# Performance work log

Hardware: AMD Instinct MI355X
Metric: run time of the kernel (lower is better)

## Reference

```python
import jax, jax.numpy as jnp
import numpy as np

EMBEDDING_DIM = 256
NUM_EMBEDDINGS = 8192
COMMITMENT_COST = 0.25
DECAY = 0.99
EPSILON = 1e-5


def setup_inputs() -> dict:
    key = jax.random.key(0)
    k1, k2 = jax.random.split(key)
    inputs = jax.random.normal(k1, (16, 32, 32, EMBEDDING_DIM), dtype=jnp.float32)
    # VarianceScaling(distribution='uniform'), fan_in scaling over [D, K]
    limit = float(np.sqrt(3.0 / EMBEDDING_DIM))
    embeddings = jax.random.uniform(k2, (EMBEDDING_DIM, NUM_EMBEDDINGS),
                                    minval=-limit, maxval=limit, dtype=jnp.float32)
    return {
        'inputs': inputs,
        'embeddings': embeddings,
        'ema_cs_hidden': jnp.zeros((NUM_EMBEDDINGS,), jnp.float32),
        'ema_dw_hidden': embeddings,  # hk initializes ema_dw to the embeddings
        'counter': 0,
        'is_training': 1,
    }


def reference(inputs, embeddings, ema_cs_hidden, ema_dw_hidden, counter, is_training):
    flat = inputs.reshape(-1, EMBEDDING_DIM)                        # [N, D]
    distances = (jnp.sum(flat ** 2, axis=1, keepdims=True)
                 - 2.0 * (flat @ embeddings)
                 + jnp.sum(embeddings ** 2, axis=0, keepdims=True))  # [N, K]
    encoding_indices = jnp.argmax(-distances, axis=1)                # [N]
    encodings = jax.nn.one_hot(encoding_indices, NUM_EMBEDDINGS,
                               dtype=distances.dtype)                # [N, K]
    idx = encoding_indices.reshape(inputs.shape[:-1])
    quantized = embeddings.T[idx]                                    # gather codebook
    e_latent_loss = jnp.mean((jax.lax.stop_gradient(quantized) - inputs) ** 2)
    loss = COMMITMENT_COST * e_latent_loss

    if is_training:
        # haiku ExponentialMovingAverage with zero-debias
        new_counter = counter + 1
        debias = 1.0 - DECAY ** new_counter
        cs_hidden = ema_cs_hidden * DECAY + jnp.sum(encodings, axis=0) * (1.0 - DECAY)
        cs_avg = cs_hidden / debias                                  # [K]
        dw = flat.T @ encodings                                      # [D, K] scatter-add as GEMM
        dw_hidden = ema_dw_hidden * DECAY + dw * (1.0 - DECAY)
        dw_avg = dw_hidden / debias
        n = jnp.sum(cs_avg)
        cs_norm = (cs_avg + EPSILON) / (n + NUM_EMBEDDINGS * EPSILON) * n
        new_embeddings = dw_avg / cs_norm[None, :]                   # [D, K]
    else:
        new_embeddings = embeddings

    # straight-through estimator
    quantized_st = inputs + jax.lax.stop_gradient(quantized - inputs)
    avg_probs = jnp.mean(encodings, axis=0)
    perplexity = jnp.exp(-jnp.sum(avg_probs * jnp.log(avg_probs + 1e-10)))
    return (quantized_st, loss, perplexity, idx, new_embeddings)
```

## Files before the change

kernel.cpp:

```cpp
#include <hip/hip_runtime.h>
#include <math.h>

#define DD 256
#define KK 8192
#define NN 16384
#define DECAYF 0.99f
#define EPSF 1e-5f
#define TAU 4e-3f

#define O_Q    0
#define O_LOSS 4194304
#define O_PERP 4194305
#define O_IDX  4194306
#define O_EMB  4210690

typedef float f32x4 __attribute__((ext_vector_type(4)));
typedef _Float16 f16x8 __attribute__((ext_vector_type(8)));

__device__ __forceinline__ unsigned short f2h(float f) {
  union { _Float16 h; unsigned short u; } c;
  c.h = (_Float16)f;
  return c.u;
}

__device__ __forceinline__ void gll16(const void* g, void* l) {
  __builtin_amdgcn_global_load_lds((const __attribute__((address_space(1))) void*)g,
                                   (__attribute__((address_space(3))) void*)l, 16, 0, 0);
}

__global__ void k_convert_x(const float* __restrict__ x, unsigned short* __restrict__ Ah,
                            float* __restrict__ esq) {
  int i = blockIdx.x * 256 + threadIdx.x;
  if (blockIdx.x < 32) esq[blockIdx.x * 256 + threadIdx.x] = 0.f;
  float4 v = ((const float4*)x)[i];
  ushort4 h;
  h.x = f2h(v.x); h.y = f2h(v.y); h.z = f2h(v.z); h.w = f2h(v.w);
  ((ushort4*)Ah)[i] = h;
}

__global__ void k_convert_e(const float* __restrict__ emb, unsigned short* __restrict__ Eh,
                            float* __restrict__ embT, float* __restrict__ esq) {
  __shared__ float ld[32 * 33];
  int t = threadIdx.x;
  int k0 = blockIdx.x * 32, d0 = blockIdx.y * 32;
  {
    int din = t >> 3, kq = (t & 7) * 4;
    float4 v = *(const float4*)(emb + (size_t)(d0 + din) * KK + k0 + kq);
    ld[din * 33 + kq + 0] = v.x; ld[din * 33 + kq + 1] = v.y;
    ld[din * 33 + kq + 2] = v.z; ld[din * 33 + kq + 3] = v.w;
  }
  __syncthreads();
  int kout = t >> 3, dq = (t & 7) * 4;
  float f0 = ld[(dq + 0) * 33 + kout], f1 = ld[(dq + 1) * 33 + kout];
  float f2 = ld[(dq + 2) * 33 + kout], f3 = ld[(dq + 3) * 33 + kout];
  size_t o = (size_t)(k0 + kout) * DD + d0 + dq;
  float4 fv; fv.x = f0; fv.y = f1; fv.z = f2; fv.w = f3;
  *(float4*)(embT + o) = fv;
  ushort4 hv;
  hv.x = f2h(f0); hv.y = f2h(f1); hv.z = f2h(f2); hv.w = f2h(f3);
  *(ushort4*)(Eh + o) = hv;
  float p = (f0 * f0 + f1 * f1) + (f2 * f2 + f3 * f3);
  p += __shfl_xor(p, 1, 64);
  p += __shfl_xor(p, 2, 64);
  p += __shfl_xor(p, 4, 64);
  if ((t & 7) == 0) atomicAdd(esq + k0 + kout, p);
}

__global__ void k_zero(float4* __restrict__ p) {
  p[(size_t)blockIdx.x * 256 + threadIdx.x] = make_float4(0.f, 0.f, 0.f, 0.f);
}

__launch_bounds__(256, 2)
__global__ void k_dist_mfma(const unsigned short* __restrict__ Ah, const unsigned short* __restrict__ Bh,
                            const float* __restrict__ esq,
                            float* __restrict__ part1, float* __restrict__ part2,
                            int* __restrict__ partidx) {
  __shared__ __align__(16) unsigned short sA[8192];
  __shared__ __align__(16) unsigned short sB[8192];

  const int tid = threadIdx.x;
  const int w = tid >> 6, lane = tid & 63;
  const int kb = blockIdx.x, nb = blockIdx.y;
  const int row0 = nb * 128, col0 = kb * 128;

  size_t gA[4], gB[4];
  int lbase[4];
  #pragma unroll
  for (int s = 0; s < 4; ++s) {
    int r = (w * 4 + s) * 8 + (lane >> 3);
    int c = (lane & 7) ^ (r & 7);
    gA[s] = (size_t)(row0 + r) * DD + c * 8;
    gB[s] = (size_t)(col0 + r) * DD + c * 8;
    lbase[s] = (w * 4 + s) * 512;
  }
  const int m = lane & 15, q = lane >> 4;

  f32x4 acc[2][8];
  #pragma unroll
  for (int i = 0; i < 2; ++i)
    #pragma unroll
    for (int j = 0; j < 8; ++j) acc[i][j] = (f32x4)0.f;

  for (int it = 0; it < 4; ++it) {
    const int d0 = it * 64;
    __syncthreads();
    #pragma unroll
    for (int s = 0; s < 4; ++s) {
      gll16(Ah + gA[s] + d0, sA + lbase[s]);
      gll16(Bh + gB[s] + d0, sB + lbase[s]);
    }
    __syncthreads();
    #pragma unroll
    for (int kk = 0; kk < 2; ++kk) {
      f16x8 a[2];
      #pragma unroll
      for (int i = 0; i < 2; ++i) {
        int wr = w * 32 + i * 16 + m;
        int slot = (kk * 4 + q) ^ (wr & 7);
        a[i] = *(const f16x8*)(sA + wr * 64 + slot * 8);
      }
      #pragma unroll
      for (int j = 0; j < 8; ++j) {
        int cn = j * 16 + m;
        int slot = (kk * 4 + q) ^ (cn & 7);
        f16x8 b = *(const f16x8*)(sB + cn * 64 + slot * 8);
        acc[0][j] = __builtin_amdgcn_mfma_f32_16x16x32_f16(a[0], b, acc[0][j], 0, 0, 0);
        acc[1][j] = __builtin_amdgcn_mfma_f32_16x16x32_f16(a[1], b, acc[1][j], 0, 0, 0);
      }
    }
  }

  float eq[8];
  #pragma unroll
  for (int j = 0; j < 8; ++j) eq[j] = esq[col0 + j * 16 + m];

  #pragma unroll
  for (int i = 0; i < 2; ++i) {
    #pragma unroll
    for (int reg = 0; reg < 4; ++reg) {
      float m1 = 3.402823466e+38f, m2 = 3.402823466e+38f;
      int bi = 0;
      #pragma unroll
      for (int j = 0; j < 8; ++j) {
        float dd = fmaf(-2.0f, acc[i][j][reg], eq[j]);
        if (dd < m1) { m2 = m1; m1 = dd; bi = col0 + j * 16 + m; }
        else if (dd < m2) m2 = dd;
      }
      #pragma unroll
      for (int st = 1; st < 16; st <<= 1) {
        float ov = __shfl_xor(m1, st, 64);
        int   oi = __shfl_xor(bi, st, 64);
        float o2 = __shfl_xor(m2, st, 64);
        float big = fmaxf(m1, ov);
        m2 = fminf(fminf(m2, o2), big);
        if (ov < m1 || (ov == m1 && oi < bi)) { m1 = ov; bi = oi; }
      }
      if (m == 0) {
        int prow = row0 + w * 32 + i * 16 + q * 4 + reg;
        int pidx = prow * 64 + kb;
        part1[pidx] = m1; part2[pidx] = m2; partidx[pidx] = bi;
      }
    }
  }
}

__global__ void k_argmin2(const float* __restrict__ part1, const float* __restrict__ part2,
                          const int* __restrict__ partidx, int* __restrict__ idxw,
                          int* __restrict__ listc, int* __restrict__ list) {
  int w = threadIdx.x >> 6, l = threadIdx.x & 63;
  int row = blockIdx.x * 4 + w;
  int base = row * 64 + l;
  float m1 = part1[base], m2 = part2[base];
  int bi = partidx[base];
  #pragma unroll
  for (int st = 1; st < 64; st <<= 1) {
    float ov = __shfl_xor(m1, st, 64);
    int   oi = __shfl_xor(bi, st, 64);
    float o2 = __shfl_xor(m2, st, 64);
    float big = fmaxf(m1, ov);
    m2 = fminf(fminf(m2, o2), big);
    if (ov < m1 || (ov == m1 && oi < bi)) { m1 = ov; bi = oi; }
  }
  if (l == 0) {
    idxw[row] = bi;
    if (m2 - m1 < TAU) { int pos = atomicAdd(listc, 1); list[pos] = row; }
  }
}

__global__ void k_rescore(const float* __restrict__ x, const float* __restrict__ emb,
                          const int* __restrict__ listc, const int* __restrict__ list,
                          unsigned long long* __restrict__ keys) {
  __shared__ float se[8192];
  __shared__ double red[256];
  const int t = threadIdx.x;
  const int k0 = blockIdx.x * 32;
  #pragma unroll
  for (int i = 0; i < 32; ++i) {
    int elem = i * 256 + t;
    int d = elem >> 5, c = elem & 31;
    se[d * 32 + c] = emb[(size_t)d * KK + k0 + c];
  }
  __syncthreads();
  const int c = t & 31, p = t >> 5;
  int cnt = *listc;
  for (int li = blockIdx.y; li < cnt; li += gridDim.y) {
    int row = list[li];
    const float* xr = x + (size_t)row * DD;
    double acc = 0.0;
    #pragma unroll
    for (int j = 0; j < 32; ++j) {
      int d = p * 32 + j;
      double df = (double)xr[d] - (double)se[d * 32 + c];
      acc = fma(df, df, acc);
    }
    red[c * 8 + p] = acc;
    __syncthreads();
    if (t < 64) {
      unsigned long long key = ~0ull;
      if (t < 32) {
        double dist = 0.0;
        #pragma unroll
        for (int qq = 0; qq < 8; ++qq) dist += red[t * 8 + qq];
        key = ((unsigned long long)__double_as_longlong(dist) & ~0x1FFFull)
              | (unsigned long long)(k0 + t);
      }
      #pragma unroll
      for (int s = 1; s < 64; s <<= 1) {
        unsigned long long o = __shfl_xor(key, s, 64);
        if (o < key) key = o;
      }
      if (t == 0) atomicMin(&keys[row], key);
    }
    __syncthreads();
  }
}

__global__ void k_gather(const float* __restrict__ x, const float* __restrict__ embT,
                         const int* __restrict__ idxw, const unsigned long long* __restrict__ keys,
                         const int* __restrict__ train,
                         float* __restrict__ outq, float* __restrict__ outidx,
                         float* __restrict__ dwT, float* __restrict__ counts,
                         float* __restrict__ loss_part) {
  int w = threadIdx.x >> 6, l = threadIdx.x & 63;
  int n = blockIdx.x * 4 + w;
  unsigned long long kv = keys[n];
  int k = (kv != ~0ull) ? (int)(kv & 0x1FFFull) : idxw[n];
  float4 xv = ((const float4*)(x + (size_t)n * DD))[l];
  float4 qv = ((const float4*)(embT + (size_t)k * DD))[l];
  int d = l * 4;

  ((float4*)(outq + (size_t)n * DD))[l] = qv;

  float e0 = qv.x - xv.x, e1 = qv.y - xv.y, e2 = qv.z - xv.z, e3 = qv.w - xv.w;
  float ls = (e0 * e0 + e1 * e1) + (e2 * e2 + e3 * e3);

  if (*train) {
    const float wdw = 1.0f - DECAYF;
    float* base = dwT + (size_t)k * DD + d;
    atomicAdd(base + 0, xv.x * wdw);
    atomicAdd(base + 1, xv.y * wdw);
    atomicAdd(base + 2, xv.z * wdw);
    atomicAdd(base + 3, xv.w * wdw);
  }

  #pragma unroll
  for (int s = 1; s < 64; s <<= 1) ls += __shfl_xor(ls, s, 64);
  if (l == 0) {
    atomicAdd(&loss_part[blockIdx.x & 255], ls);
    atomicAdd(&counts[k], 1.0f);
    outidx[n] = (float)k;
  }
}

__global__ void k_stats(const float* __restrict__ counts, const float* __restrict__ ema_cs,
                        const int* __restrict__ counter, const int* __restrict__ train,
                        const float* __restrict__ loss_part, float* __restrict__ csn,
                        float* __restrict__ outloss, float* __restrict__ outperp) {
  __shared__ float s_n[4], s_e[4], s_l[4], s_tot[1];
  int tid = threadIdx.x;
  float debias = 1.0f - powf(DECAYF, (float)(*counter + 1));
  float nloc = 0.f, eloc = 0.f;
  float lloc = loss_part[tid];
  float avg[32];
  for (int i = 0; i < 32; ++i) {
    int k = tid + i * 256;
    float c = counts[k];
    float h = ema_cs[k] * DECAYF + c * (1.0f - DECAYF);
    float a = h / debias;
    avg[i] = a;
    nloc += a;
    float p = c * (1.0f / 16384.0f);
    eloc += p * logf(p + 1e-10f);
  }
  #pragma unroll
  for (int s = 1; s < 64; s <<= 1) {
    nloc += __shfl_xor(nloc, s, 64);
    eloc += __shfl_xor(eloc, s, 64);
    lloc += __shfl_xor(lloc, s, 64);
  }
  int w = tid >> 6, lane = tid & 63;
  if (lane == 0) { s_n[w] = nloc; s_e[w] = eloc; s_l[w] = lloc; }
  __syncthreads();
  if (tid == 0) {
    float nt = (s_n[0] + s_n[1]) + (s_n[2] + s_n[3]);
    float et = (s_e[0] + s_e[1]) + (s_e[2] + s_e[3]);
    float lt = (s_l[0] + s_l[1]) + (s_l[2] + s_l[3]);
    s_tot[0] = nt;
    outperp[0] = expf(-et);
    outloss[0] = 0.25f * (lt / 4194304.0f);
  }
  __syncthreads();
  float nsum = s_tot[0];
  float denom = nsum + 8192.0f * EPSF;
  for (int i = 0; i < 32; ++i) {
    int k = tid + i * 256;
    csn[k] = (avg[i] + EPSF) / denom * nsum;
  }
}

__global__ void k_final(const float* __restrict__ dwT, const float* __restrict__ ema_dw,
                        const float* __restrict__ emb, const float* __restrict__ csn,
                        const int* __restrict__ counter, const int* __restrict__ train,
                        float* __restrict__ out4) {
  __shared__ float ld[32 * 33];
  int t = threadIdx.x;
  int k0 = blockIdx.x * 32, d0 = blockIdx.y * 32;
  if (*train) {
    {
      int ki = t >> 3, dq = (t & 7) * 4;
      float4 v = *(const float4*)(dwT + (size_t)(k0 + ki) * DD + d0 + dq);
      ld[ki * 33 + dq + 0] = v.x; ld[ki * 33 + dq + 1] = v.y;
      ld[ki * 33 + dq + 2] = v.z; ld[ki * 33 + dq + 3] = v.w;
    }
    __syncthreads();
    int dout = t >> 3, kq = (t & 7) * 4;
    size_t o = (size_t)(d0 + dout) * KK + k0 + kq;
    float4 e = *(const float4*)(ema_dw + o);
    float4 c = *(const float4*)(csn + k0 + kq);
    float inv = 1.0f / (1.0f - powf(DECAYF, (float)(*counter + 1)));
    float4 r;
    r.x = fmaf(e.x, DECAYF, ld[(kq + 0) * 33 + dout]) * inv / c.x;
    r.y = fmaf(e.y, DECAYF, ld[(kq + 1) * 33 + dout]) * inv / c.y;
    r.z = fmaf(e.z, DECAYF, ld[(kq + 2) * 33 + dout]) * inv / c.z;
    r.w = fmaf(e.w, DECAYF, ld[(kq + 3) * 33 + dout]) * inv / c.w;
    *(float4*)(out4 + o) = r;
  } else {
    int dout = t >> 3, kq = (t & 7) * 4;
    size_t o = (size_t)(d0 + dout) * KK + k0 + kq;
    *(float4*)(out4 + o) = *(const float4*)(emb + o);
  }
}

extern "C" void kernel_launch(void* const* d_in, const int* in_sizes, int n_in,
                              void* d_out, int out_size, void* d_ws, size_t ws_size,
                              hipStream_t stream) {
  (void)in_sizes; (void)n_in; (void)out_size; (void)ws_size;
  const float* x      = (const float*)d_in[0];
  const float* emb    = (const float*)d_in[1];
  const float* ema_cs = (const float*)d_in[2];
  const float* ema_dw = (const float*)d_in[3];
  const int*   counter = (const int*)d_in[4];
  const int*   train   = (const int*)d_in[5];

  float* out = (float*)d_out;
  float* outq    = out + O_Q;
  float* outloss = out + O_LOSS;
  float* outperp = out + O_PERP;
  float* outidx  = out + O_IDX;
  float* out4    = out + O_EMB;

  char* W = (char*)d_ws;
  unsigned short* Ah   = (unsigned short*)(W);
  unsigned short* Eh   = (unsigned short*)(W + 8388608);
  float* embT          = (float*)(W + 12582912);
  float* part1         = (float*)(W + 20971520);
  float* part2         = (float*)(W + 25165824);
  int*   partidx       = (int*)(W + 29360128);
  float* dwT           = part1;
  unsigned long long* keys = (unsigned long long*)(W + 33554432);
  float* esq           = (float*)(W + 33685504);
  float* csn           = (float*)(W + 33718272);
  float* counts        = (float*)(W + 33751040);
  float* loss_part     = (float*)(W + 33783808);
  int*   listc         = (int*)(W + 33784832);
  int*   list          = (int*)(W + 33784836);
  int*   idxw          = (int*)(W + 33850372);

  hipMemsetAsync(counts, 0, 32768 + 1024 + 4, stream);
  hipMemsetAsync(keys, 0xFF, NN * sizeof(unsigned long long), stream);

  k_convert_x<<<4096, 256, 0, stream>>>(x, Ah, esq);
  k_convert_e<<<dim3(256, 8), 256, 0, stream>>>(emb, Eh, embT, esq);
  k_dist_mfma<<<dim3(64, 128), 256, 0, stream>>>(Ah, Eh, esq, part1, part2, partidx);
  k_argmin2<<<4096, 256, 0, stream>>>(part1, part2, partidx, idxw, listc, list);
  k_zero<<<2048, 256, 0, stream>>>((float4*)dwT);
  k_rescore<<<dim3(256, 8), 256, 0, stream>>>(x, emb, listc, list, keys);
  k_gather<<<4096, 256, 0, stream>>>(x, embT, idxw, keys, train, outq, outidx, dwT, counts, loss_part);
  k_stats<<<1, 256, 0, stream>>>(counts, ema_cs, counter, train, loss_part, csn, outloss, outperp);
  k_final<<<dim3(256, 8), 256, 0, stream>>>(dwT, ema_dw, emb, csn, counter, train, out4);
}
```

Before: 400.7 us.

## Fuse conversion kernels, drop zero kernel, load A fragments directly from global

Merges the x and embedding conversion kernels into one launch. The separate zero kernel for dwT goes away: k_argmin2 now clears part1/part2 after reading them, and one memset zeroes esq and the small stats buffers. In the distance GEMM, each wave loads its A fragments straight from global memory into registers instead of staging them through LDS, which halves shared memory per block. The top-2 argmin updates become branchless min/max/select. The cost is uncoalesced-ish global loads for A and a change in tie-breaking, which now keeps the first-seen index rather than the lowest index on exact ties.

```diff
diff --git a/kernel.cpp b/kernel.cpp
--- a/kernel.cpp
+++ b/kernel.cpp
@@ -28,21 +28,22 @@
                                    (__attribute__((address_space(3))) void*)l, 16, 0, 0);
 }
 
-__global__ void k_convert_x(const float* __restrict__ x, unsigned short* __restrict__ Ah,
-                            float* __restrict__ esq) {
-  int i = blockIdx.x * 256 + threadIdx.x;
-  if (blockIdx.x < 32) esq[blockIdx.x * 256 + threadIdx.x] = 0.f;
-  float4 v = ((const float4*)x)[i];
-  ushort4 h;
-  h.x = f2h(v.x); h.y = f2h(v.y); h.z = f2h(v.z); h.w = f2h(v.w);
-  ((ushort4*)Ah)[i] = h;
-}
-
-__global__ void k_convert_e(const float* __restrict__ emb, unsigned short* __restrict__ Eh,
-                            float* __restrict__ embT, float* __restrict__ esq) {
+__global__ void k_convert_xe(const float* __restrict__ x, unsigned short* __restrict__ Ah,
+                             const float* __restrict__ emb, unsigned short* __restrict__ Eh,
+                             float* __restrict__ embT, float* __restrict__ esq) {
   __shared__ float ld[32 * 33];
+  int bx = blockIdx.x;
   int t = threadIdx.x;
-  int k0 = blockIdx.x * 32, d0 = blockIdx.y * 32;
+  if (bx < 4096) {
+    int i = bx * 256 + t;
+    float4 v = ((const float4*)x)[i];
+    ushort4 h;
+    h.x = f2h(v.x); h.y = f2h(v.y); h.z = f2h(v.z); h.w = f2h(v.w);
+    ((ushort4*)Ah)[i] = h;
+    return;
+  }
+  int eb = bx - 4096;
+  int k0 = (eb & 255) * 32, d0 = (eb >> 8) * 32;
   {
     int din = t >> 3, kq = (t & 7) * 4;
     float4 v = *(const float4*)(emb + (size_t)(d0 + din) * KK + k0 + kq);
@@ -66,34 +67,32 @@
   if ((t & 7) == 0) atomicAdd(esq + k0 + kout, p);
 }
 
-__global__ void k_zero(float4* __restrict__ p) {
-  p[(size_t)blockIdx.x * 256 + threadIdx.x] = make_float4(0.f, 0.f, 0.f, 0.f);
-}
-
 __launch_bounds__(256, 2)
 __global__ void k_dist_mfma(const unsigned short* __restrict__ Ah, const unsigned short* __restrict__ Bh,
                             const float* __restrict__ esq,
                             float* __restrict__ part1, float* __restrict__ part2,
                             int* __restrict__ partidx) {
-  __shared__ __align__(16) unsigned short sA[8192];
   __shared__ __align__(16) unsigned short sB[8192];
 
   const int tid = threadIdx.x;
   const int w = tid >> 6, lane = tid & 63;
   const int kb = blockIdx.x, nb = blockIdx.y;
   const int row0 = nb * 128, col0 = kb * 128;
-
-  size_t gA[4], gB[4];
-  int lbase[4];
+  const int m = lane & 15, q = lane >> 4;
+
+  size_t gB[4];
+  int lbB[4];
   #pragma unroll
   for (int s = 0; s < 4; ++s) {
-    int r = (w * 4 + s) * 8 + (lane >> 3);
+    int g = w * 4 + s;
+    int r = g * 8 + (lane >> 3);
     int c = (lane & 7) ^ (r & 7);
-    gA[s] = (size_t)(row0 + r) * DD + c * 8;
     gB[s] = (size_t)(col0 + r) * DD + c * 8;
-    lbase[s] = (w * 4 + s) * 512;
-  }
-  const int m = lane & 15, q = lane >> 4;
+    lbB[s] = g * 512;
+  }
+
+  const unsigned short* pA0 = Ah + (size_t)(row0 + w * 32 + m) * DD + q * 8;
+  const unsigned short* pA1 = pA0 + 16 * DD;
 
   f32x4 acc[2][8];
   #pragma unroll
@@ -105,27 +104,23 @@
     const int d0 = it * 64;
     __syncthreads();
     #pragma unroll
-    for (int s = 0; s < 4; ++s) {
-      gll16(Ah + gA[s] + d0, sA + lbase[s]);
-      gll16(Bh + gB[s] + d0, sB + lbase[s]);
+    for (int s = 0; s < 4; ++s) gll16(Bh + gB[s] + d0, sB + lbB[s]);
+    f16x8 a[2][2];
+    #pragma unroll
+    for (int kk = 0; kk < 2; ++kk) {
+      a[kk][0] = *(const f16x8*)(pA0 + d0 + kk * 32);
+      a[kk][1] = *(const f16x8*)(pA1 + d0 + kk * 32);
     }
     __syncthreads();
     #pragma unroll
     for (int kk = 0; kk < 2; ++kk) {
-      f16x8 a[2];
-      #pragma unroll
-      for (int i = 0; i < 2; ++i) {
-        int wr = w * 32 + i * 16 + m;
-        int slot = (kk * 4 + q) ^ (wr & 7);
-        a[i] = *(const f16x8*)(sA + wr * 64 + slot * 8);
-      }
       #pragma unroll
       for (int j = 0; j < 8; ++j) {
         int cn = j * 16 + m;
         int slot = (kk * 4 + q) ^ (cn & 7);
         f16x8 b = *(const f16x8*)(sB + cn * 64 + slot * 8);
-        acc[0][j] = __builtin_amdgcn_mfma_f32_16x16x32_f16(a[0], b, acc[0][j], 0, 0, 0);
-        acc[1][j] = __builtin_amdgcn_mfma_f32_16x16x32_f16(a[1], b, acc[1][j], 0, 0, 0);
+        acc[0][j] = __builtin_amdgcn_mfma_f32_16x16x32_f16(a[kk][0], b, acc[0][j], 0, 0, 0);
+        acc[1][j] = __builtin_amdgcn_mfma_f32_16x16x32_f16(a[kk][1], b, acc[1][j], 0, 0, 0);
       }
     }
   }
@@ -143,17 +138,20 @@
       #pragma unroll
       for (int j = 0; j < 8; ++j) {
         float dd = fmaf(-2.0f, acc[i][j][reg], eq[j]);
-        if (dd < m1) { m2 = m1; m1 = dd; bi = col0 + j * 16 + m; }
-        else if (dd < m2) m2 = dd;
+        bool p = dd < m1;
+        m2 = fminf(m2, fmaxf(dd, m1));
+        m1 = fminf(m1, dd);
+        bi = p ? (col0 + j * 16 + m) : bi;
       }
       #pragma unroll
       for (int st = 1; st < 16; st <<= 1) {
         float ov = __shfl_xor(m1, st, 64);
         int   oi = __shfl_xor(bi, st, 64);
         float o2 = __shfl_xor(m2, st, 64);
-        float big = fmaxf(m1, ov);
-        m2 = fminf(fminf(m2, o2), big);
-        if (ov < m1 || (ov == m1 && oi < bi)) { m1 = ov; bi = oi; }
+        m2 = fminf(fminf(m2, o2), fmaxf(m1, ov));
+        bool p = ov < m1;
+        m1 = fminf(m1, ov);
+        bi = p ? oi : bi;
       }
       if (m == 0) {
         int prow = row0 + w * 32 + i * 16 + q * 4 + reg;
@@ -164,22 +162,25 @@
   }
 }
 
-__global__ void k_argmin2(const float* __restrict__ part1, const float* __restrict__ part2,
+__global__ void k_argmin2(float* __restrict__ part1, float* __restrict__ part2,
                           const int* __restrict__ partidx, int* __restrict__ idxw,
                           int* __restrict__ listc, int* __restrict__ list) {
   int w = threadIdx.x >> 6, l = threadIdx.x & 63;
   int row = blockIdx.x * 4 + w;
-  int base = row * 64 + l;
-  float m1 = part1[base], m2 = part2[base];
-  int bi = partidx[base];
+  int f = blockIdx.x * 256 + threadIdx.x;
+  float m1 = part1[f], m2 = part2[f];
+  int bi = partidx[f];
+  part1[f] = 0.f;
+  part2[f] = 0.f;
   #pragma unroll
   for (int st = 1; st < 64; st <<= 1) {
     float ov = __shfl_xor(m1, st, 64);
     int   oi = __shfl_xor(bi, st, 64);
     float o2 = __shfl_xor(m2, st, 64);
-    float big = fmaxf(m1, ov);
-    m2 = fminf(fminf(m2, o2), big);
-    if (ov < m1 || (ov == m1 && oi < bi)) { m1 = ov; bi = oi; }
+    m2 = fminf(fminf(m2, o2), fmaxf(m1, ov));
+    bool p = ov < m1;
+    m1 = fminf(m1, ov);
+    bi = p ? oi : bi;
   }
   if (l == 0) {
     idxw[row] = bi;
@@ -386,14 +387,12 @@
   int*   list          = (int*)(W + 33784836);
   int*   idxw          = (int*)(W + 33850372);
 
-  hipMemsetAsync(counts, 0, 32768 + 1024 + 4, stream);
+  hipMemsetAsync(esq, 0, 99332, stream);
   hipMemsetAsync(keys, 0xFF, NN * sizeof(unsigned long long), stream);
 
-  k_convert_x<<<4096, 256, 0, stream>>>(x, Ah, esq);
-  k_convert_e<<<dim3(256, 8), 256, 0, stream>>>(emb, Eh, embT, esq);
+  k_convert_xe<<<6144, 256, 0, stream>>>(x, Ah, emb, Eh, embT, esq);
   k_dist_mfma<<<dim3(64, 128), 256, 0, stream>>>(Ah, Eh, esq, part1, part2, partidx);
   k_argmin2<<<4096, 256, 0, stream>>>(part1, part2, partidx, idxw, listc, list);
-  k_zero<<<2048, 256, 0, stream>>>((float4*)dwT);
   k_rescore<<<dim3(256, 8), 256, 0, stream>>>(x, emb, listc, list, keys);
   k_gather<<<4096, 256, 0, stream>>>(x, embT, idxw, keys, train, outq, outidx, dwT, counts, loss_part);
   k_stats<<<1, 256, 0, stream>>>(counts, ema_cs, counter, train, loss_part, csn, outloss, outperp);
```

New measurement: 370.1 us. 1.08x faster.
